# Kernel tuning notes

Measured on AMD Instinct MI355X. Metric: run time of the kernel, lower is better.

## Reference

```python
import jax, jax.numpy as jnp
import numpy as np

N, E, F, H, L = 50000, 800000, 128, 128, 64

def _xavier(key, shape):
    a = np.sqrt(6.0 / (shape[0] + shape[1]))
    return jax.random.uniform(key, shape, jnp.float32, -a, a)

def setup_inputs() -> dict:
    key = jax.random.key(0)
    ks = jax.random.split(key, 20)
    inp = {
        "x": jax.random.normal(ks[0], (N, F), jnp.float32),
        "edge_index": jax.random.randint(ks[1], (2, E), 0, N),
        "edge_weight": jax.random.uniform(ks[2], (E, 2), jnp.float32),
    }
    dims = [(F, H), (H, 2 * L), (L, H), (H, F)]
    for i, (din, dout) in enumerate(dims, start=1):
        inp[f"c{i}_Wc"] = _xavier(ks[2 + 3 * i], (din + 2, din))
        inp[f"c{i}_bc"] = jnp.zeros((din,), jnp.float32)
        inp[f"c{i}_W"] = _xavier(ks[3 + 3 * i], (din, dout))
        inp[f"c{i}_b"] = jnp.zeros((dout,), jnp.float32)
    inp["et_W"] = _xavier(ks[18], (F + 2, 1))
    inp["et_b"] = jnp.zeros((1,), jnp.float32)
    return inp

def _conv(x, src, dst, ew, Wc, bc, W, b):
    # gather x_j, fuse edge-feature MLP (Linear+ReLU), scatter-mean by dst, Bayesian matmul (eval: mu)
    m = jax.nn.relu(jnp.concatenate([x[src], ew], axis=-1) @ Wc + bc)  # [E, din]
    agg = jax.ops.segment_sum(m, dst, num_segments=N)                  # [N, din]
    cnt = jax.ops.segment_sum(jnp.ones((E, 1), m.dtype), dst, num_segments=N)
    out = agg / jnp.maximum(cnt, 1.0)                                  # scatter-mean
    return out @ W + b

def reference(x, edge_index, edge_weight,
              c1_Wc, c1_bc, c1_W, c1_b,
              c2_Wc, c2_bc, c2_W, c2_b,
              c3_Wc, c3_bc, c3_W, c3_b,
              c4_Wc, c4_bc, c4_W, c4_b,
              et_W, et_b):
    src, dst = edge_index[0], edge_index[1]
    h = jax.nn.relu(_conv(x, src, dst, edge_weight, c1_Wc, c1_bc, c1_W, c1_b))
    h = jax.nn.relu(_conv(h, src, dst, edge_weight, c2_Wc, c2_bc, c2_W, c2_b))
    mu, logvar = h[:, :L], h[:, L:]
    z = mu  # eval-mode reparametrize
    edge_feat = jnp.concatenate([jnp.abs(x[src] - x[dst]), edge_weight], axis=-1)
    pet = edge_feat @ et_W + et_b  # [E, 1]
    d = jax.nn.relu(_conv(z, src, dst, edge_weight, c3_Wc, c3_bc, c3_W, c3_b))
    recon = jnp.tanh(_conv(d, src, dst, edge_weight, c4_Wc, c4_bc, c4_W, c4_b))
    return (recon, mu, logvar, pet)
```

## Files before the change

kernel.cpp:

```cpp
#include <hip/hip_runtime.h>
#include <hip/hip_bf16.h>

#define NN 50000
#define NE 800000

typedef __bf16 bf16x8 __attribute__((ext_vector_type(8)));
typedef float f32x4 __attribute__((ext_vector_type(4)));

__device__ __forceinline__ unsigned short f2bu(float f) {
    return __builtin_bit_cast(unsigned short, (__bf16)f);
}
__device__ __forceinline__ float b2f(unsigned short u) {
    return (float)__builtin_bit_cast(__bf16, u);
}

__global__ void k_cvt(const float* __restrict__ x, unsigned short* __restrict__ xb, int n8) {
    int i = blockIdx.x * blockDim.x + threadIdx.x;
    if (i >= n8) return;
    float4 a = ((const float4*)x)[i * 2];
    float4 b = ((const float4*)x)[i * 2 + 1];
    bf16x8 v;
    v[0] = (__bf16)a.x; v[1] = (__bf16)a.y; v[2] = (__bf16)a.z; v[3] = (__bf16)a.w;
    v[4] = (__bf16)b.x; v[5] = (__bf16)b.y; v[6] = (__bf16)b.z; v[7] = (__bf16)b.w;
    ((uint4*)xb)[i] = __builtin_bit_cast(uint4, v);
}

__global__ void k_deg(const int* __restrict__ ei, int* __restrict__ deg, int E) {
    int e = blockIdx.x * blockDim.x + threadIdx.x;
    if (e < E) atomicAdd(&deg[ei[E + e]], 1);
}

__global__ __launch_bounds__(256)
void k_scan1(const int* __restrict__ deg, int* __restrict__ part, int n) {
    const int b = blockIdx.x, t = threadIdx.x;
    const int chunk = (n + gridDim.x - 1) / gridDim.x;
    const int lo = b * chunk;
    const int cnt = min(chunk, n - lo);
    int v = (t < cnt) ? deg[lo + t] : 0;
    v += __shfl_xor(v, 1); v += __shfl_xor(v, 2); v += __shfl_xor(v, 4);
    v += __shfl_xor(v, 8); v += __shfl_xor(v, 16); v += __shfl_xor(v, 32);
    __shared__ int red[4];
    if ((t & 63) == 0) red[t >> 6] = v;
    __syncthreads();
    if (t == 0) part[b] = red[0] + red[1] + red[2] + red[3];
}

__global__ __launch_bounds__(256)
void k_scan2(int* __restrict__ part) {
    __shared__ int tmp[256];
    const int t = threadIdx.x;
    const int v = part[t];
    tmp[t] = v;
    __syncthreads();
    int val = v;
    for (int off = 1; off < 256; off <<= 1) {
        int y = (t >= off) ? tmp[t - off] : 0;
        __syncthreads();
        val += y;
        tmp[t] = val;
        __syncthreads();
    }
    part[t] = val - v;
}

__global__ __launch_bounds__(256)
void k_scan3(const int* __restrict__ deg, const int* __restrict__ part,
             int* __restrict__ cursor, int n) {
    __shared__ int tmp[256];
    const int b = blockIdx.x, t = threadIdx.x;
    const int chunk = (n + gridDim.x - 1) / gridDim.x;
    const int lo = b * chunk;
    const int cnt = min(chunk, n - lo);
    const int v = (t < cnt) ? deg[lo + t] : 0;
    tmp[t] = v;
    __syncthreads();
    int val = v;
    for (int off = 1; off < 256; off <<= 1) {
        int y = (t >= off) ? tmp[t - off] : 0;
        __syncthreads();
        val += y;
        tmp[t] = val;
        __syncthreads();
    }
    if (t < cnt) cursor[lo + t] = part[b] + val - v;
}

__global__ void k_scatter(const int* __restrict__ ei, const float* __restrict__ ew,
                          int* __restrict__ cursor, int4* __restrict__ edgeS, int E) {
    int e = blockIdx.x * blockDim.x + threadIdx.x;
    if (e >= E) return;
    int d = ei[E + e];
    int s = atomicAdd(&cursor[d], 1);
    float2 w = ((const float2*)ew)[e];
    int packed = (int)((unsigned int)f2bu(w.x) | ((unsigned int)f2bu(w.y) << 16));
    edgeS[s] = make_int4(ei[e], packed, e, 0);
}

template<int KP, int NOUT, int MOUT>
__global__ __launch_bounds__(256, 2)
void k_dense(const unsigned short* __restrict__ Xb, const float* __restrict__ W,
             const float* __restrict__ bias, float* __restrict__ o0,
             float* __restrict__ o1, unsigned short* __restrict__ bo, int M)
{
    constexpr int CH = KP / 8;
    constexpr int KSTEPS = KP / 32;
    constexpr int FM = 4;
    constexpr int FN = NOUT / 32;
    constexpr int BLK = 520;

    __shared__ unsigned short Alds[8 * KSTEPS * BLK];

    const int tid = threadIdx.x;
    const int lane = tid & 63;
    const int w = tid >> 6;
    const int lrow = lane & 15;
    const int lkg = lane >> 4;
    const int wrow0 = (w >> 1) * 64;
    const int cb0 = (w & 1) * (NOUT / 2);

    bf16x8 bfr[KSTEPS][FN];
    float eb[FN];
#pragma unroll
    for (int nf = 0; nf < FN; ++nf) {
        int col = cb0 + nf * 16 + lrow;
#pragma unroll
        for (int ks = 0; ks < KSTEPS; ++ks)
#pragma unroll
            for (int j = 0; j < 8; ++j) {
                int k = ks * 32 + lkg * 8 + j;
                bfr[ks][nf][j] = (__bf16)W[k * NOUT + col];
            }
        if constexpr (MOUT != 0) eb[nf] = bias[col];
        else eb[nf] = 0.f;
    }

    const int ntiles = (M + 127) / 128;
    for (int tile = blockIdx.x; tile < ntiles; tile += gridDim.x) {
        const int base = tile * 128;
        __syncthreads();
        for (int t = tid; t < 128 * CH; t += 256) {
            int row = t / CH;
            int c = t % CH;
            int r = base + row;
            uint4 val = make_uint4(0, 0, 0, 0);
            if (r < M) val = *((const uint4*)(Xb + (size_t)r * KP) + c);
            int mb = row >> 4, lr = row & 15, ks = c >> 2, q = c & 3;
            int unit = (q * 16 + lr) ^ (q << 1);
            *(uint4*)&Alds[(mb * KSTEPS + ks) * BLK + unit * 8] = val;
        }
        __syncthreads();

        f32x4 acc[FM][FN];
#pragma unroll
        for (int mf = 0; mf < FM; ++mf)
#pragma unroll
            for (int nf = 0; nf < FN; ++nf)
                acc[mf][nf] = 0;

        const int runit = lane ^ (lkg << 1);
#pragma unroll
        for (int ks = 0; ks < KSTEPS; ++ks) {
            bf16x8 afr[FM];
#pragma unroll
            for (int mf = 0; mf < FM; ++mf) {
                int mb = (wrow0 >> 4) + mf;
                afr[mf] = *(const bf16x8*)&Alds[(mb * KSTEPS + ks) * BLK + runit * 8];
            }
#pragma unroll
            for (int mf = 0; mf < FM; ++mf)
#pragma unroll
                for (int nf = 0; nf < FN; ++nf)
                    acc[mf][nf] = __builtin_amdgcn_mfma_f32_16x16x32_bf16(
                        afr[mf], bfr[ks][nf], acc[mf][nf], 0, 0, 0);
        }

#pragma unroll
        for (int mf = 0; mf < FM; ++mf) {
#pragma unroll
            for (int reg = 0; reg < 4; ++reg) {
                int row = wrow0 + mf * 16 + lkg * 4 + reg;
                int r = base + row;
                if (r < M) {
#pragma unroll
                    for (int nf = 0; nf < FN; ++nf) {
                        int col = cb0 + nf * 16 + lrow;
                        float tv = acc[mf][nf][reg] + eb[nf];
                        if constexpr (MOUT == 0) {
                            bo[(size_t)r * NOUT + col] = f2bu(tv);
                        } else if constexpr (MOUT == 1) {
                            bo[(size_t)r * NOUT + col] = f2bu(fmaxf(tv, 0.f));
                        } else if constexpr (MOUT == 2) {
                            float v = fmaxf(tv, 0.f);
                            if (col < 64) {
                                o0[(size_t)r * 64 + col] = v;
                                bo[(size_t)r * 64 + col] = f2bu(v);
                            } else {
                                o1[(size_t)r * 64 + (col - 64)] = v;
                            }
                        } else {
                            o0[(size_t)r * NOUT + col] = tanhf(tv);
                        }
                    }
                }
            }
        }
    }
}

template<int NOUT>
__global__ __launch_bounds__(256)
void k_agg(const unsigned short* __restrict__ Yb, const int4* __restrict__ edgeS,
           const float* __restrict__ er, const float* __restrict__ bc,
           const int* __restrict__ cursor, const int* __restrict__ deg,
           unsigned short* __restrict__ meanb, int NV)
{
    constexpr int LPN = NOUT / 8;
    constexpr int NPB = 256 / LPN;
    const int tid = threadIdx.x;
    const int lg = tid % LPN;
    const int slot = tid / LPN;
    const int n = blockIdx.x * NPB + slot;
    if (n >= NV) return;
    const int c0 = lg * 8;

    float e0[8], e1[8], bcv[8], acc[8];
#pragma unroll
    for (int v = 0; v < 8; ++v) {
        e0[v] = er[c0 + v];
        e1[v] = er[NOUT + c0 + v];
        bcv[v] = bc[c0 + v];
        acc[v] = 0.f;
    }

    const int len = deg[n];
    const int base = cursor[n] - len;

    auto accum = [&](uint4 yv, int packed) {
        bf16x8 yb = __builtin_bit_cast(bf16x8, yv);
        float wx = b2f((unsigned short)(packed & 0xffff));
        float wy = b2f((unsigned short)((unsigned int)packed >> 16));
#pragma unroll
        for (int v = 0; v < 8; ++v)
            acc[v] += fmaxf((float)yb[v] + wx * e0[v] + wy * e1[v] + bcv[v], 0.f);
    };

    const int nfull = len >> 2;
    int i = base;
    for (int c = 0; c < nfull; ++c, i += 4) {
        int4 p0 = edgeS[i], p1 = edgeS[i + 1], p2 = edgeS[i + 2], p3 = edgeS[i + 3];
        uint4 y0 = *(const uint4*)(Yb + (size_t)p0.x * NOUT + c0);
        uint4 y1 = *(const uint4*)(Yb + (size_t)p1.x * NOUT + c0);
        uint4 y2 = *(const uint4*)(Yb + (size_t)p2.x * NOUT + c0);
        uint4 y3 = *(const uint4*)(Yb + (size_t)p3.x * NOUT + c0);
        accum(y0, p0.y);
        accum(y1, p1.y);
        accum(y2, p2.y);
        accum(y3, p3.y);
    }
    for (; i < base + len; ++i) {
        int4 p0 = edgeS[i];
        uint4 y0 = *(const uint4*)(Yb + (size_t)p0.x * NOUT + c0);
        accum(y0, p0.y);
    }

    const float inv = 1.f / (float)(len > 1 ? len : 1);
    bf16x8 ov;
#pragma unroll
    for (int v = 0; v < 8; ++v) ov[v] = (__bf16)(acc[v] * inv);
    *(uint4*)(meanb + (size_t)n * NOUT + c0) = __builtin_bit_cast(uint4, ov);
}

__global__ __launch_bounds__(256)
void k_pet2(const unsigned short* __restrict__ xb, const int4* __restrict__ edgeS,
            const int* __restrict__ cursor, const int* __restrict__ deg,
            const float* __restrict__ etW, const float* __restrict__ etb,
            float* __restrict__ out, int NV)
{
    const int tid = threadIdx.x;
    const int lg = tid & 15;
    const int slot = tid >> 4;
    const int n = blockIdx.x * 16 + slot;
    if (n >= NV) return;
    const int c0 = lg * 8;

    float xd[8], wv[8];
    {
        uint4 dv = *(const uint4*)(xb + (size_t)n * 128 + c0);
        bf16x8 dbv = __builtin_bit_cast(bf16x8, dv);
#pragma unroll
        for (int v = 0; v < 8; ++v) { xd[v] = (float)dbv[v]; wv[v] = etW[c0 + v]; }
    }
    const float w128 = etW[128], w129 = etW[129], bb = etb[0];

    const int len = deg[n];
    const int base = cursor[n] - len;

    auto edge_val = [&](uint4 sv) {
        bf16x8 sb = __builtin_bit_cast(bf16x8, sv);
        float a = 0.f;
#pragma unroll
        for (int v = 0; v < 8; ++v)
            a += fabsf((float)sb[v] - xd[v]) * wv[v];
        a += __shfl_xor(a, 1);
        a += __shfl_xor(a, 2);
        a += __shfl_xor(a, 4);
        a += __shfl_xor(a, 8);
        return a;
    };
    auto emit = [&](int4 p, float a) {
        if (lg == 0) {
            float wx = b2f((unsigned short)(p.y & 0xffff));
            float wy = b2f((unsigned short)((unsigned int)p.y >> 16));
            out[p.z] = a + wx * w128 + wy * w129 + bb;
        }
    };

    const int nfull = len >> 2;
    int i = base;
    for (int c = 0; c < nfull; ++c, i += 4) {
        int4 p0 = edgeS[i], p1 = edgeS[i + 1], p2 = edgeS[i + 2], p3 = edgeS[i + 3];
        uint4 s0 = *(const uint4*)(xb + (size_t)p0.x * 128 + c0);
        uint4 s1 = *(const uint4*)(xb + (size_t)p1.x * 128 + c0);
        uint4 s2 = *(const uint4*)(xb + (size_t)p2.x * 128 + c0);
        uint4 s3 = *(const uint4*)(xb + (size_t)p3.x * 128 + c0);
        emit(p0, edge_val(s0));
        emit(p1, edge_val(s1));
        emit(p2, edge_val(s2));
        emit(p3, edge_val(s3));
    }
    for (; i < base + len; ++i) {
        int4 p0 = edgeS[i];
        uint4 s0 = *(const uint4*)(xb + (size_t)p0.x * 128 + c0);
        emit(p0, edge_val(s0));
    }
}

extern "C" void kernel_launch(void* const* d_in, const int* in_sizes, int n_in,
                              void* d_out, int out_size, void* d_ws, size_t ws_size,
                              hipStream_t stream) {
    const float* x   = (const float*)d_in[0];
    const int*   ei  = (const int*)d_in[1];
    const float* ew  = (const float*)d_in[2];
    const float* Wc1 = (const float*)d_in[3];
    const float* bc1 = (const float*)d_in[4];
    const float* W1  = (const float*)d_in[5];
    const float* b1  = (const float*)d_in[6];
    const float* Wc2 = (const float*)d_in[7];
    const float* bc2 = (const float*)d_in[8];
    const float* W2  = (const float*)d_in[9];
    const float* b2  = (const float*)d_in[10];
    const float* Wc3 = (const float*)d_in[11];
    const float* bc3 = (const float*)d_in[12];
    const float* W3  = (const float*)d_in[13];
    const float* b3  = (const float*)d_in[14];
    const float* Wc4 = (const float*)d_in[15];
    const float* bc4 = (const float*)d_in[16];
    const float* W4  = (const float*)d_in[17];
    const float* b4  = (const float*)d_in[18];
    const float* etW = (const float*)d_in[19];
    const float* etb = (const float*)d_in[20];

    float* out   = (float*)d_out;
    float* recon = out;
    float* mu    = out + (size_t)NN * 128;
    float* lv    = mu + (size_t)NN * 64;
    float* pet   = lv + (size_t)NN * 64;

    char* wsp = (char*)d_ws;
    unsigned short* xb  = (unsigned short*)(wsp);
    unsigned short* Yb  = (unsigned short*)(wsp + 12800000);
    unsigned short* ab  = (unsigned short*)(wsp + 25600000);
    unsigned short* h1b = (unsigned short*)(wsp + 38400000);
    unsigned short* zb  = (unsigned short*)(wsp + 51200000);
    unsigned short* db  = (unsigned short*)(wsp + 57600000);
    int* deg            = (int*)(wsp + 70400000);
    int* cursor         = (int*)(wsp + 70600000);
    int4* edgeS         = (int4*)(wsp + 70800000);
    int* part           = (int*)(wsp + 83600000);

    const int E = NE, NV = NN;

    hipMemsetAsync(deg, 0, NV * sizeof(int), stream);
    k_deg<<<(E + 255) / 256, 256, 0, stream>>>(ei, deg, E);
    k_scan1<<<256, 256, 0, stream>>>(deg, part, NV);
    k_scan2<<<1, 256, 0, stream>>>(part);
    k_scan3<<<256, 256, 0, stream>>>(deg, part, cursor, NV);
    k_scatter<<<(E + 255) / 256, 256, 0, stream>>>(ei, ew, cursor, edgeS, E);
    k_cvt<<<(800000 + 255) / 256, 256, 0, stream>>>(x, xb, 800000);

    k_dense<128, 128, 0><<<391, 256, 0, stream>>>(xb, Wc1, nullptr,
                                                  nullptr, nullptr, Yb, NV);
    k_agg<128><<<(NV + 15) / 16, 256, 0, stream>>>(Yb, edgeS, Wc1 + 128 * 128, bc1,
                                                   cursor, deg, ab, NV);
    k_dense<128, 128, 1><<<391, 256, 0, stream>>>(ab, W1, b1,
                                                  nullptr, nullptr, h1b, NV);

    k_dense<128, 128, 0><<<391, 256, 0, stream>>>(h1b, Wc2, nullptr,
                                                  nullptr, nullptr, Yb, NV);
    k_agg<128><<<(NV + 15) / 16, 256, 0, stream>>>(Yb, edgeS, Wc2 + 128 * 128, bc2,
                                                   cursor, deg, ab, NV);
    k_dense<128, 128, 2><<<391, 256, 0, stream>>>(ab, W2, b2,
                                                  mu, lv, zb, NV);

    k_pet2<<<(NV + 15) / 16, 256, 0, stream>>>(xb, edgeS, cursor, deg,
                                               etW, etb, pet, NV);

    k_dense<64, 64, 0><<<391, 256, 0, stream>>>(zb, Wc3, nullptr,
                                                nullptr, nullptr, Yb, NV);
    k_agg<64><<<(NV + 31) / 32, 256, 0, stream>>>(Yb, edgeS, Wc3 + 64 * 64, bc3,
                                                  cursor, deg, ab, NV);
    k_dense<64, 128, 1><<<391, 256, 0, stream>>>(ab, W3, b3,
                                                 nullptr, nullptr, db, NV);

    k_dense<128, 128, 0><<<391, 256, 0, stream>>>(db, Wc4, nullptr,
                                                  nullptr, nullptr, Yb, NV);
    k_agg<128><<<(NV + 15) / 16, 256, 0, stream>>>(Yb, edgeS, Wc4 + 128 * 128, bc4,
                                                   cursor, deg, ab, NV);
    k_dense<128, 128, 3><<<391, 256, 0, stream>>>(ab, W4, b4,
                                                  recon, nullptr, nullptr, NV);
}
```

Before: 382.9 us.

## Shrink CSR edge records to int2 and write pet through a rank permutation

Packs each sorted edge record into int2 (source, packed weights) instead of int4, halving the edge-list bytes read by every aggregation pass. The original edge id moves into a separate rank array written during scatter. The pet kernel now writes coalesced results in sorted order to a temporary buffer, and a new permutation kernel gathers them back into original edge order. This adds one extra pass and a small rank write, in exchange for less traffic in the four aggregations and no scattered stores in pet.

```diff
diff --git a/kernel.cpp b/kernel.cpp
--- a/kernel.cpp
+++ b/kernel.cpp
@@ -86,14 +86,16 @@
 }
 
 __global__ void k_scatter(const int* __restrict__ ei, const float* __restrict__ ew,
-                          int* __restrict__ cursor, int4* __restrict__ edgeS, int E) {
+                          int* __restrict__ cursor, int2* __restrict__ edgeS,
+                          int* __restrict__ rank, int E) {
     int e = blockIdx.x * blockDim.x + threadIdx.x;
     if (e >= E) return;
     int d = ei[E + e];
     int s = atomicAdd(&cursor[d], 1);
     float2 w = ((const float2*)ew)[e];
     int packed = (int)((unsigned int)f2bu(w.x) | ((unsigned int)f2bu(w.y) << 16));
-    edgeS[s] = make_int4(ei[e], packed, e, 0);
+    edgeS[s] = make_int2(ei[e], packed);
+    rank[e] = s;
 }
 
 template<int KP, int NOUT, int MOUT>
@@ -209,7 +211,7 @@
 
 template<int NOUT>
 __global__ __launch_bounds__(256)
-void k_agg(const unsigned short* __restrict__ Yb, const int4* __restrict__ edgeS,
+void k_agg(const unsigned short* __restrict__ Yb, const int2* __restrict__ edgeS,
            const float* __restrict__ er, const float* __restrict__ bc,
            const int* __restrict__ cursor, const int* __restrict__ deg,
            unsigned short* __restrict__ meanb, int NV)
@@ -247,7 +249,7 @@
     const int nfull = len >> 2;
     int i = base;
     for (int c = 0; c < nfull; ++c, i += 4) {
-        int4 p0 = edgeS[i], p1 = edgeS[i + 1], p2 = edgeS[i + 2], p3 = edgeS[i + 3];
+        int2 p0 = edgeS[i], p1 = edgeS[i + 1], p2 = edgeS[i + 2], p3 = edgeS[i + 3];
         uint4 y0 = *(const uint4*)(Yb + (size_t)p0.x * NOUT + c0);
         uint4 y1 = *(const uint4*)(Yb + (size_t)p1.x * NOUT + c0);
         uint4 y2 = *(const uint4*)(Yb + (size_t)p2.x * NOUT + c0);
@@ -258,7 +260,7 @@
         accum(y3, p3.y);
     }
     for (; i < base + len; ++i) {
-        int4 p0 = edgeS[i];
+        int2 p0 = edgeS[i];
         uint4 y0 = *(const uint4*)(Yb + (size_t)p0.x * NOUT + c0);
         accum(y0, p0.y);
     }
@@ -271,10 +273,10 @@
 }
 
 __global__ __launch_bounds__(256)
-void k_pet2(const unsigned short* __restrict__ xb, const int4* __restrict__ edgeS,
+void k_petS(const unsigned short* __restrict__ xb, const int2* __restrict__ edgeS,
             const int* __restrict__ cursor, const int* __restrict__ deg,
             const float* __restrict__ etW, const float* __restrict__ etb,
-            float* __restrict__ out, int NV)
+            float* __restrict__ tmp, int NV)
 {
     const int tid = threadIdx.x;
     const int lg = tid & 15;
@@ -307,32 +309,38 @@
         a += __shfl_xor(a, 8);
         return a;
     };
-    auto emit = [&](int4 p, float a) {
+    auto emit = [&](int i, int2 p, float a) {
         if (lg == 0) {
             float wx = b2f((unsigned short)(p.y & 0xffff));
             float wy = b2f((unsigned short)((unsigned int)p.y >> 16));
-            out[p.z] = a + wx * w128 + wy * w129 + bb;
+            tmp[i] = a + wx * w128 + wy * w129 + bb;
         }
     };
 
     const int nfull = len >> 2;
     int i = base;
     for (int c = 0; c < nfull; ++c, i += 4) {
-        int4 p0 = edgeS[i], p1 = edgeS[i + 1], p2 = edgeS[i + 2], p3 = edgeS[i + 3];
+        int2 p0 = edgeS[i], p1 = edgeS[i + 1], p2 = edgeS[i + 2], p3 = edgeS[i + 3];
         uint4 s0 = *(const uint4*)(xb + (size_t)p0.x * 128 + c0);
         uint4 s1 = *(const uint4*)(xb + (size_t)p1.x * 128 + c0);
         uint4 s2 = *(const uint4*)(xb + (size_t)p2.x * 128 + c0);
         uint4 s3 = *(const uint4*)(xb + (size_t)p3.x * 128 + c0);
-        emit(p0, edge_val(s0));
-        emit(p1, edge_val(s1));
-        emit(p2, edge_val(s2));
-        emit(p3, edge_val(s3));
+        emit(i,     p0, edge_val(s0));
+        emit(i + 1, p1, edge_val(s1));
+        emit(i + 2, p2, edge_val(s2));
+        emit(i + 3, p3, edge_val(s3));
     }
     for (; i < base + len; ++i) {
-        int4 p0 = edgeS[i];
+        int2 p0 = edgeS[i];
         uint4 s0 = *(const uint4*)(xb + (size_t)p0.x * 128 + c0);
-        emit(p0, edge_val(s0));
-    }
+        emit(i, p0, edge_val(s0));
+    }
+}
+
+__global__ void k_petP(const float* __restrict__ tmp, const int* __restrict__ rank,
+                       float* __restrict__ out, int E) {
+    int e = blockIdx.x * blockDim.x + threadIdx.x;
+    if (e < E) out[e] = tmp[rank[e]];
 }
 
 extern "C" void kernel_launch(void* const* d_in, const int* in_sizes, int n_in,
@@ -375,7 +383,9 @@
     unsigned short* db  = (unsigned short*)(wsp + 57600000);
     int* deg            = (int*)(wsp + 70400000);
     int* cursor         = (int*)(wsp + 70600000);
-    int4* edgeS         = (int4*)(wsp + 70800000);
+    int2* edgeS         = (int2*)(wsp + 70800000);
+    int* rank           = (int*)(wsp + 77200000);
+    float* tmpP         = (float*)(wsp + 80400000);
     int* part           = (int*)(wsp + 83600000);
 
     const int E = NE, NV = NN;
@@ -385,7 +395,7 @@
     k_scan1<<<256, 256, 0, stream>>>(deg, part, NV);
     k_scan2<<<1, 256, 0, stream>>>(part);
     k_scan3<<<256, 256, 0, stream>>>(deg, part, cursor, NV);
-    k_scatter<<<(E + 255) / 256, 256, 0, stream>>>(ei, ew, cursor, edgeS, E);
+    k_scatter<<<(E + 255) / 256, 256, 0, stream>>>(ei, ew, cursor, edgeS, rank, E);
     k_cvt<<<(800000 + 255) / 256, 256, 0, stream>>>(x, xb, 800000);
 
     k_dense<128, 128, 0><<<391, 256, 0, stream>>>(xb, Wc1, nullptr,
@@ -402,8 +412,9 @@
     k_dense<128, 128, 2><<<391, 256, 0, stream>>>(ab, W2, b2,
                                                   mu, lv, zb, NV);
 
-    k_pet2<<<(NV + 15) / 16, 256, 0, stream>>>(xb, edgeS, cursor, deg,
-                                               etW, etb, pet, NV);
+    k_petS<<<(NV + 15) / 16, 256, 0, stream>>>(xb, edgeS, cursor, deg,
+                                               etW, etb, tmpP, NV);
+    k_petP<<<(E + 255) / 256, 256, 0, stream>>>(tmpP, rank, pet, E);
 
     k_dense<64, 64, 0><<<391, 256, 0, stream>>>(zb, Wc3, nullptr,
                                                 nullptr, nullptr, Yb, NV);
```

Result: no change. 389.3 us (+1.7%).
